# Optimization experiments

Hardware: AMD Instinct MI355X
Metric: run time of the kernel (lower is better)

## Reference

```python
import jax, jax.numpy as jnp
import numpy as np

B, N, C, H = 4, 2048, 1024, 16
D = C // H  # head_dim = 64


def setup_inputs() -> dict:
    key = jax.random.key(0)
    ks = jax.random.split(key, 11)
    s = 1.0 / np.sqrt(C)
    return {
        "query": jax.random.normal(ks[0], (B, N, C), jnp.float32),
        "key": jax.random.normal(ks[1], (B, N, C), jnp.float32),
        "value": jax.random.normal(ks[2], (B, N, C), jnp.float32),
        "Wq": jax.random.normal(ks[3], (C, C), jnp.float32) * s,
        "bq": jax.random.normal(ks[4], (C,), jnp.float32) * s,
        "Wk": jax.random.normal(ks[5], (C, C), jnp.float32) * s,
        "bk": jax.random.normal(ks[6], (C,), jnp.float32) * s,
        "Wv": jax.random.normal(ks[7], (C, C), jnp.float32) * s,
        "bv": jax.random.normal(ks[8], (C,), jnp.float32) * s,
        "Wp": jax.random.normal(ks[9], (C, C), jnp.float32) * s,
        "bp": jax.random.normal(ks[10], (C,), jnp.float32) * s,
    }


def _split_heads(x):
    # [B, N, C] -> [B, H, N, D]
    return x.reshape(B, N, H, D).transpose(0, 2, 1, 3)


def reference(query, key, value, Wq, bq, Wk, bk, Wv, bv, Wp, bp):
    q = _split_heads(query @ Wq + bq)  # [B,H,N,D]
    k = _split_heads(key @ Wk + bk)
    v = _split_heads(value @ Wv + bv)

    # custom additive frequency bias over key positions (broadcast over B,H,Tq)
    freq_range = jnp.linspace(0.0, 1.0, N, dtype=query.dtype)
    freq_bias = -((freq_range - 0.5) ** 2) * 10.0  # [N]

    scale = 1.0 / jnp.sqrt(jnp.asarray(D, query.dtype))
    att = jnp.einsum('bhqd,bhkd->bhqk', q * scale, k)  # [B,H,N,N]
    att = att + freq_bias[None, None, None, :]
    att = jax.nn.softmax(att, axis=-1)
    y = jnp.einsum('bhqk,bhkd->bhqd', att, v)  # [B,H,N,D]

    y = y.transpose(0, 2, 1, 3).reshape(B, N, C)
    out = y @ Wp + bp
    return out
```

## Files before the change

kernel.cpp:

```cpp
#include <hip/hip_runtime.h>
#include <stdint.h>

typedef unsigned short u16;
typedef float f32x4 __attribute__((ext_vector_type(4)));
typedef float f32x16 __attribute__((ext_vector_type(16)));
typedef __bf16 bf16x8 __attribute__((ext_vector_type(8)));
typedef u16 u16x8 __attribute__((ext_vector_type(8)));
typedef u16 u16x4 __attribute__((ext_vector_type(4)));

#define B_ 4
#define N_ 2048
#define C_ 1024
#define H_ 16
#define D_ 64

__device__ __forceinline__ u16 f2bf(float f) {
  unsigned u = __builtin_bit_cast(unsigned, f);
  u += 0x7FFFu + ((u >> 16) & 1u);
  return (u16)(u >> 16);
}
__device__ __forceinline__ float bf2f(u16 h) {
  unsigned u = ((unsigned)h) << 16;
  return __builtin_bit_cast(float, u);
}
__device__ __forceinline__ f32x4 mfma16(u16x8 a, u16x8 b, f32x4 c) {
  return __builtin_amdgcn_mfma_f32_16x16x32_bf16(
      __builtin_bit_cast(bf16x8, a), __builtin_bit_cast(bf16x8, b), c, 0, 0, 0);
}
__device__ __forceinline__ f32x16 mfma32(u16x8 a, u16x8 b, f32x16 c) {
  return __builtin_amdgcn_mfma_f32_32x32x16_bf16(
      __builtin_bit_cast(bf16x8, a), __builtin_bit_cast(bf16x8, b), c, 0, 0, 0);
}
__device__ __forceinline__ void gload_lds16(const void* g, void* l) {
  __builtin_amdgcn_global_load_lds(
      (const __attribute__((address_space(1))) void*)g,
      (__attribute__((address_space(3))) void*)l, 16, 0, 0);
}
__device__ __forceinline__ float exp2_hw(float x) {
  return __builtin_amdgcn_exp2f(x);
}
__device__ __forceinline__ unsigned cvt_pk_bf16(float lo, float hi) {
  unsigned d;
  asm("v_cvt_pk_bf16_f32 %0, %1, %2" : "=v"(d) : "v"(lo), "v"(hi));
  return d;
}

__global__ __launch_bounds__(256) void convert_x(const float* __restrict__ in,
                                                 u16* __restrict__ out, int n4) {
  int i = blockIdx.x * 256 + threadIdx.x;
  if (i >= n4) return;
  f32x4 v = *(const f32x4*)(in + (size_t)i * 4);
  u16x4 o;
#pragma unroll
  for (int j = 0; j < 4; j++) o[j] = f2bf(v[j]);
  *(u16x4*)(out + (size_t)i * 4) = o;
}

__global__ __launch_bounds__(256) void transpose_convert_w(const float* __restrict__ in,
                                                           u16* __restrict__ out) {
  __shared__ float tile[64][65];
  const int t = threadIdx.x;
  const int bx = blockIdx.x;
  const int tr = (bx >> 4) << 6;
  const int tc = (bx & 15) << 6;
#pragma unroll
  for (int i = 0; i < 16; i++) {
    int idx = i * 256 + t;
    int rr = idx >> 6, cc = idx & 63;
    tile[rr][cc] = in[(size_t)(tr + rr) * C_ + tc + cc];
  }
  __syncthreads();
#pragma unroll
  for (int i = 0; i < 16; i++) {
    int idx = i * 256 + t;
    int rr = idx >> 6, cc = idx & 63;
    out[(size_t)(tc + rr) * C_ + tr + cc] = f2bf(tile[cc][rr]);
  }
}

template <int EPI, bool SPLIT>
__global__ __launch_bounds__(256) void gemm128(
    const u16* __restrict__ A, const u16* __restrict__ A2,
    const u16* __restrict__ BT, const float* __restrict__ bias,
    void* __restrict__ outp, float scale, int M, int N, int K) {
  __shared__ u16 lA[128 * 32];
  __shared__ u16 lB[128 * 32];
  __shared__ u16 lA2[SPLIT ? 128 * 32 : 8];

  const int t = threadIdx.x;
  const int w = t >> 6;
  const int lane = t & 63;
  const int g = lane >> 4;
  const int r = lane & 15;
  const int nTn = N >> 7;
  const int tm = blockIdx.x / nTn;
  const int tn = blockIdx.x % nTn;
  const int m0 = tm << 7;
  const int n0 = tn << 7;
  const int wm = (w >> 1) << 6;
  const int wn = (w & 1) << 6;

  const int row_s = t >> 2;
  const int kc_s = (t & 3) << 3;

  f32x4 acc[4][4] = {};

  for (int k0 = 0; k0 < K; k0 += 32) {
    __syncthreads();
    {
      const u16* gA = A + (size_t)(m0 + row_s) * K + (k0 + kc_s);
      gload_lds16(gA, (char*)lA + (w << 10));
      gload_lds16(gA + (size_t)64 * K, (char*)lA + 4096 + (w << 10));
      const u16* gB = BT + (size_t)(n0 + row_s) * K + (k0 + kc_s);
      gload_lds16(gB, (char*)lB + (w << 10));
      gload_lds16(gB + (size_t)64 * K, (char*)lB + 4096 + (w << 10));
      if constexpr (SPLIT) {
        const u16* gA2 = A2 + (size_t)(m0 + row_s) * K + (k0 + kc_s);
        gload_lds16(gA2, (char*)lA2 + (w << 10));
        gload_lds16(gA2 + (size_t)64 * K, (char*)lA2 + 4096 + (w << 10));
      }
    }
    asm volatile("s_waitcnt vmcnt(0)" ::: "memory");
    __syncthreads();

    u16x8 af[4], bfv[4];
#pragma unroll
    for (int i = 0; i < 4; i++)
      af[i] = *(const u16x8*)&lA[(wm + i * 16 + r) * 32 + g * 8];
#pragma unroll
    for (int i = 0; i < 4; i++)
      bfv[i] = *(const u16x8*)&lB[(wn + i * 16 + r) * 32 + g * 8];
#pragma unroll
    for (int mi = 0; mi < 4; mi++)
#pragma unroll
      for (int ni = 0; ni < 4; ni++)
        acc[mi][ni] = mfma16(af[mi], bfv[ni], acc[mi][ni]);
    if constexpr (SPLIT) {
      u16x8 al[4];
#pragma unroll
      for (int i = 0; i < 4; i++)
        al[i] = *(const u16x8*)&lA2[(wm + i * 16 + r) * 32 + g * 8];
#pragma unroll
      for (int mi = 0; mi < 4; mi++)
#pragma unroll
        for (int ni = 0; ni < 4; ni++)
          acc[mi][ni] = mfma16(al[mi], bfv[ni], acc[mi][ni]);
    }
  }

  float bv[4];
#pragma unroll
  for (int ni = 0; ni < 4; ni++) bv[ni] = bias[n0 + wn + ni * 16 + r];

  if constexpr (EPI == 2) {
    float* out = (float*)outp;
#pragma unroll
    for (int mi = 0; mi < 4; mi++)
#pragma unroll
      for (int ni = 0; ni < 4; ni++)
#pragma unroll
        for (int j = 0; j < 4; j++) {
          int gm = m0 + wm + mi * 16 + g * 4 + j;
          int gn = n0 + wn + ni * 16 + r;
          out[(size_t)gm * N + gn] = (acc[mi][ni][j] + bv[ni]) * scale;
        }
  } else if constexpr (EPI == 0) {
    u16* out = (u16*)outp;
#pragma unroll
    for (int mi = 0; mi < 4; mi++)
#pragma unroll
      for (int ni = 0; ni < 4; ni++)
#pragma unroll
        for (int j = 0; j < 4; j++) {
          int gm = m0 + wm + mi * 16 + g * 4 + j;
          int gn = n0 + wn + ni * 16 + r;
          float v = (acc[mi][ni][j] + bv[ni]) * scale;
          int b = gm >> 11, n = gm & 2047, h = gn >> 6, d = gn & 63;
          out[((((size_t)b * H_ + h) * N_ + n) << 6) + d] = f2bf(v);
        }
  } else if constexpr (EPI == 3) {
    u16* out = (u16*)outp;
#pragma unroll
    for (int mi = 0; mi < 4; mi++)
#pragma unroll
      for (int ni = 0; ni < 4; ni++)
#pragma unroll
        for (int j = 0; j < 4; j++) {
          int gm = m0 + wm + mi * 16 + g * 4 + j;
          int gn = n0 + wn + ni * 16 + r;
          float v = acc[mi][ni][j] + bv[ni];
          int b = gm >> 11, n = gm & 2047, h = gn >> 6, d = gn & 63;
          size_t off = (((size_t)(b * H_ + h)) << 17) + ((size_t)(n >> 5) << 11) +
                       ((d >> 4) << 9) + ((((d >> 3) & 1) << 5) + (n & 31)) * 8 + (d & 7);
          out[off] = f2bf(v);
        }
  } else {
    u16* out = (u16*)outp;
#pragma unroll
    for (int mi = 0; mi < 4; mi++)
#pragma unroll
      for (int ni = 0; ni < 4; ni++) {
        int gm0 = m0 + wm + mi * 16 + g * 4;
        int gn = n0 + wn + ni * 16 + r;
        int b = gm0 >> 11, n = gm0 & 2047, h = gn >> 6, d = gn & 63;
        size_t off = (((size_t)(b * H_ + h)) << 17) + ((size_t)(n >> 6) << 12) +
                     ((size_t)((d >> 5) * 4 + ((n >> 4) & 3)) << 9) +
                     ((((n >> 3) & 1) << 5) + (d & 31)) * 8 + (n & 7);
        u16x4 pk;
#pragma unroll
        for (int j = 0; j < 4; j++) pk[j] = f2bf(acc[mi][ni][j] + bv[ni]);
        *(u16x4*)&out[off] = pk;
      }
  }
}

__device__ __forceinline__ void load_kv(const u16* __restrict__ Kb,
                                        const u16* __restrict__ Vb, int k0,
                                        int lane, u16x8 (&kf)[8], u16x8 (&vf)[8]) {
  const u16* pK = Kb + ((size_t)(k0 >> 5) << 11) + lane * 8;
#pragma unroll
  for (int s = 0; s < 4; s++) {
    kf[s] = *(const u16x8*)(pK + (s << 9));
    kf[4 + s] = *(const u16x8*)(pK + 2048 + (s << 9));
  }
  const u16* pV = Vb + ((size_t)(k0 >> 6) << 12) + lane * 8;
#pragma unroll
  for (int c = 0; c < 8; c++) vf[c] = *(const u16x8*)(pV + (c << 9));
}

__device__ __forceinline__ void attn_tile(int k0, const float* __restrict__ tbl,
                                          float* __restrict__ xlds,
                                          const u16x8 (&kf)[8], const u16x8 (&vf)[8],
                                          const u16x8 (&qf)[4], f32x16& o0, f32x16& o1,
                                          float& m_e, float& l_run, int ql, int h) {
  const float L2E = 1.44269504088896340736f;
  f32x16 st0 = {}, st1 = {};
#pragma unroll
  for (int s = 0; s < 4; s++) st0 = mfma32(kf[s], qf[s], st0);
#pragma unroll
  for (int s = 0; s < 4; s++) st1 = mfma32(kf[4 + s], qf[s], st1);

  float e0[16], e1[16];
#pragma unroll
  for (int g2 = 0; g2 < 4; g2++) {
    f32x4 t0 = *(const f32x4*)&tbl[k0 + 8 * g2 + 4 * h];
    f32x4 t1 = *(const f32x4*)&tbl[k0 + 32 + 8 * g2 + 4 * h];
#pragma unroll
    for (int jj = 0; jj < 4; jj++) {
      e0[g2 * 4 + jj] = fmaf(st0[g2 * 4 + jj], L2E, t0[jj]);
      e1[g2 * 4 + jj] = fmaf(st1[g2 * 4 + jj], L2E, t1[jj]);
    }
  }
  float mx[8];
#pragma unroll
  for (int j = 0; j < 8; j++)
    mx[j] = fmaxf(fmaxf(e0[j], e0[j + 8]), fmaxf(e1[j], e1[j + 8]));
#pragma unroll
  for (int j = 0; j < 4; j++) mx[j] = fmaxf(mx[j], mx[j + 4]);
  float pmax = fmaxf(fmaxf(mx[0], mx[1]), fmaxf(mx[2], mx[3]));
  pmax = fmaxf(pmax, __shfl_xor(pmax, 32));

  if (!__all(pmax <= m_e + 8.0f)) {
    float m_new = fmaxf(m_e, pmax);
    float resc = exp2_hw(m_e - m_new);
    xlds[ql] = resc;
#pragma unroll
    for (int g2 = 0; g2 < 4; g2++) {
      f32x4 r4 = *(const f32x4*)&xlds[8 * g2 + 4 * h];
#pragma unroll
      for (int jj = 0; jj < 4; jj++) {
        o0[g2 * 4 + jj] *= r4[jj];
        o1[g2 * 4 + jj] *= r4[jj];
      }
    }
    l_run *= resc;
    m_e = m_new;
  }

#pragma unroll
  for (int j = 0; j < 16; j++) e0[j] = exp2_hw(e0[j] - m_e);
#pragma unroll
  for (int j = 0; j < 16; j++) e1[j] = exp2_hw(e1[j] - m_e);
  float sm[8];
#pragma unroll
  for (int j = 0; j < 8; j++) sm[j] = (e0[j] + e0[j + 8]) + (e1[j] + e1[j + 8]);
#pragma unroll
  for (int j = 0; j < 4; j++) sm[j] += sm[j + 4];
  float lt = (sm[0] + sm[1]) + (sm[2] + sm[3]);
  lt += __shfl_xor(lt, 32);
  l_run += lt;

  unsigned W0[8], W1[8];
#pragma unroll
  for (int j = 0; j < 8; j++) {
    W0[j] = cvt_pk_bf16(e0[2 * j], e0[2 * j + 1]);
    W1[j] = cvt_pk_bf16(e1[2 * j], e1[2 * j + 1]);
  }
  u16x8 pa[4];
#pragma unroll
  for (int c = 0; c < 2; c++) {
    unsigned a0 = W0[4 * c], b0 = W0[4 * c + 2];
    unsigned a1 = W0[4 * c + 1], b1 = W0[4 * c + 3];
    asm("v_permlane32_swap_b32 %0, %1" : "+v"(a0), "+v"(b0));
    asm("v_permlane32_swap_b32 %0, %1" : "+v"(a1), "+v"(b1));
    union { unsigned u[4]; u16x8 v; } pk_;
    pk_.u[0] = a0; pk_.u[1] = a1; pk_.u[2] = b0; pk_.u[3] = b1;
    pa[c] = pk_.v;
  }
#pragma unroll
  for (int c = 0; c < 2; c++) {
    unsigned a0 = W1[4 * c], b0 = W1[4 * c + 2];
    unsigned a1 = W1[4 * c + 1], b1 = W1[4 * c + 3];
    asm("v_permlane32_swap_b32 %0, %1" : "+v"(a0), "+v"(b0));
    asm("v_permlane32_swap_b32 %0, %1" : "+v"(a1), "+v"(b1));
    union { unsigned u[4]; u16x8 v; } pk_;
    pk_.u[0] = a0; pk_.u[1] = a1; pk_.u[2] = b0; pk_.u[3] = b1;
    pa[2 + c] = pk_.v;
  }

#pragma unroll
  for (int cc = 0; cc < 4; cc++) {
    o0 = mfma32(pa[cc], vf[cc], o0);
    o1 = mfma32(pa[cc], vf[4 + cc], o1);
  }
}

__global__ __launch_bounds__(256) void attn_fwd(
    const u16* __restrict__ Q, const u16* __restrict__ K,
    const u16* __restrict__ VT, u16* __restrict__ yhi, u16* __restrict__ ylo) {
  __shared__ __align__(16) float tbl[N_];
  __shared__ __align__(16) float xldsa[4][32];

  const int bid0 = blockIdx.x;
  const int bid = (bid0 & 7) * 128 + (bid0 >> 3);
  const int bh = bid >> 4;
  const int qt = bid & 15;
  const int t = threadIdx.x, w = t >> 6, lane = t & 63;
  const int ql = lane & 31;
  const int h = lane >> 5;
  const float L2E = 1.44269504088896340736f;

#pragma unroll
  for (int i = 0; i < 8; i++) {
    int k = i * 256 + t;
    float tt = (float)k * (1.0f / 2047.0f) - 0.5f;
    tbl[k] = -10.0f * L2E * tt * tt;
  }
  __syncthreads();

  const int q0 = qt * 128 + w * 32;
  const u16* Qb = Q + (size_t)bh * (N_ * D_);
  const u16* Kb = K + (size_t)bh * (N_ * D_);
  const u16* Vb = VT + (size_t)bh * (D_ * N_);
  float* xlds = xldsa[w];

  u16x8 qf[4];
#pragma unroll
  for (int s = 0; s < 4; s++)
    qf[s] = *(const u16x8*)(Qb + (size_t)(q0 + ql) * D_ + s * 16 + h * 8);

  f32x16 o0 = {}, o1 = {};
  float m_e = -INFINITY, l_run = 0.f;

  u16x8 kA[8], vA[8], kB[8], vB[8];
  load_kv(Kb, Vb, 0, lane, kA, vA);

  for (int k0 = 0; k0 < N_; k0 += 128) {
    load_kv(Kb, Vb, k0 + 64, lane, kB, vB);
    attn_tile(k0, tbl, xlds, kA, vA, qf, o0, o1, m_e, l_run, ql, h);
    if (k0 + 128 < N_)
      load_kv(Kb, Vb, k0 + 128, lane, kA, vA);
    attn_tile(k0 + 64, tbl, xlds, kB, vB, qf, o0, o1, m_e, l_run, ql, h);
  }

  float linv = 1.0f / l_run;
  xlds[ql] = linv;
  const int b = bh >> 4, hh = bh & 15;
#pragma unroll
  for (int g2 = 0; g2 < 4; g2++) {
    f32x4 r4 = *(const f32x4*)&xlds[8 * g2 + 4 * h];
#pragma unroll
    for (int jj = 0; jj < 4; jj++) {
      int q = q0 + 8 * g2 + 4 * h + jj;
      size_t base = ((size_t)b * N_ + q) * C_ + hh * 64;
      float v0 = o0[g2 * 4 + jj] * r4[jj];
      float v1 = o1[g2 * 4 + jj] * r4[jj];
      u16 h0 = f2bf(v0), h1 = f2bf(v1);
      yhi[base + ql] = h0;
      ylo[base + ql] = f2bf(v0 - bf2f(h0));
      yhi[base + 32 + ql] = h1;
      ylo[base + 32 + ql] = f2bf(v1 - bf2f(h1));
    }
  }
}

extern "C" void kernel_launch(void* const* d_in, const int* in_sizes, int n_in,
                              void* d_out, int out_size, void* d_ws, size_t ws_size,
                              hipStream_t stream) {
  (void)in_sizes; (void)n_in; (void)out_size; (void)ws_size;
  const float* q_in = (const float*)d_in[0];
  const float* k_in = (const float*)d_in[1];
  const float* v_in = (const float*)d_in[2];
  const float* Wq = (const float*)d_in[3];
  const float* bq = (const float*)d_in[4];
  const float* Wk = (const float*)d_in[5];
  const float* bk = (const float*)d_in[6];
  const float* Wv = (const float*)d_in[7];
  const float* bv = (const float*)d_in[8];
  const float* Wp = (const float*)d_in[9];
  const float* bp = (const float*)d_in[10];

  char* ws = (char*)d_ws;
  const size_t SZ_X = (size_t)8192 * 1024 * sizeof(u16);
  const size_t SZ_W = (size_t)1024 * 1024 * sizeof(u16);
  u16* Xq = (u16*)(ws);
  u16* Xk = (u16*)(ws + SZ_X);
  u16* Xv = (u16*)(ws + 2 * SZ_X);
  u16* Qb = (u16*)(ws + 3 * SZ_X);
  u16* Kb = (u16*)(ws + 4 * SZ_X);
  u16* VT = (u16*)(ws + 5 * SZ_X);
  u16* WqT = (u16*)(ws + 6 * SZ_X);
  u16* WkT = (u16*)(ws + 6 * SZ_X + SZ_W);
  u16* WvT = (u16*)(ws + 6 * SZ_X + 2 * SZ_W);
  u16* WpT = (u16*)(ws + 6 * SZ_X + 3 * SZ_W);
  u16* Yhi = Xq;
  u16* Ylo = Xk;

  convert_x<<<8192, 256, 0, stream>>>(q_in, Xq, 2097152);
  convert_x<<<8192, 256, 0, stream>>>(k_in, Xk, 2097152);
  convert_x<<<8192, 256, 0, stream>>>(v_in, Xv, 2097152);
  transpose_convert_w<<<256, 256, 0, stream>>>(Wq, WqT);
  transpose_convert_w<<<256, 256, 0, stream>>>(Wk, WkT);
  transpose_convert_w<<<256, 256, 0, stream>>>(Wv, WvT);
  transpose_convert_w<<<256, 256, 0, stream>>>(Wp, WpT);

  gemm128<0, false><<<512, 256, 0, stream>>>(Xq, nullptr, WqT, bq, Qb, 0.125f, 8192, 1024, 1024);
  gemm128<3, false><<<512, 256, 0, stream>>>(Xk, nullptr, WkT, bk, Kb, 1.0f, 8192, 1024, 1024);
  gemm128<1, false><<<512, 256, 0, stream>>>(Xv, nullptr, WvT, bv, VT, 1.0f, 8192, 1024, 1024);

  attn_fwd<<<1024, 256, 0, stream>>>(Qb, Kb, VT, Yhi, Ylo);

  gemm128<2, true><<<512, 256, 0, stream>>>(Yhi, Ylo, WpT, bp, (float*)d_out, 1.0f, 8192, 1024, 1024);
}
```

Measured before the change: 292.5 us.

## Double GEMM K-tile to 64 with XOR-swizzled LDS and batch conversion launches

The projection GEMM now stages a 64-wide K slice per iteration instead of 32. This halves the number of barrier and wait cycles per output tile and gives more MFMA work per sync. The LDS layout uses an XOR swizzle on 16-byte chunks to avoid bank conflicts on the wider 128-byte rows. The input conversion and weight transpose kernels are also merged into single multi-plane launches (3 and 4 planes) to cut launch count. The cost is more LDS per block, which may reduce occupancy for the split variant.

```diff
diff --git a/kernel.cpp b/kernel.cpp
--- a/kernel.cpp
+++ b/kernel.cpp
@@ -45,10 +45,13 @@
   return d;
 }
 
-__global__ __launch_bounds__(256) void convert_x(const float* __restrict__ in,
-                                                 u16* __restrict__ out, int n4) {
+__global__ __launch_bounds__(256) void convert_x3(
+    const float* __restrict__ a, const float* __restrict__ b,
+    const float* __restrict__ c, u16* __restrict__ oa, u16* __restrict__ ob,
+    u16* __restrict__ oc) {
+  const float* in = blockIdx.y == 0 ? a : (blockIdx.y == 1 ? b : c);
+  u16* out = blockIdx.y == 0 ? oa : (blockIdx.y == 1 ? ob : oc);
   int i = blockIdx.x * 256 + threadIdx.x;
-  if (i >= n4) return;
   f32x4 v = *(const f32x4*)(in + (size_t)i * 4);
   u16x4 o;
 #pragma unroll
@@ -56,8 +59,15 @@
   *(u16x4*)(out + (size_t)i * 4) = o;
 }
 
-__global__ __launch_bounds__(256) void transpose_convert_w(const float* __restrict__ in,
-                                                           u16* __restrict__ out) {
+__global__ __launch_bounds__(256) void transpose_convert_w4(
+    const float* __restrict__ w0, const float* __restrict__ w1,
+    const float* __restrict__ w2, const float* __restrict__ w3,
+    u16* __restrict__ o0, u16* __restrict__ o1, u16* __restrict__ o2,
+    u16* __restrict__ o3) {
+  const float* in = blockIdx.y == 0 ? w0
+                    : blockIdx.y == 1 ? w1
+                    : blockIdx.y == 2 ? w2 : w3;
+  u16* out = blockIdx.y == 0 ? o0 : blockIdx.y == 1 ? o1 : blockIdx.y == 2 ? o2 : o3;
   __shared__ float tile[64][65];
   const int t = threadIdx.x;
   const int bx = blockIdx.x;
@@ -83,9 +93,9 @@
     const u16* __restrict__ A, const u16* __restrict__ A2,
     const u16* __restrict__ BT, const float* __restrict__ bias,
     void* __restrict__ outp, float scale, int M, int N, int K) {
-  __shared__ u16 lA[128 * 32];
-  __shared__ u16 lB[128 * 32];
-  __shared__ u16 lA2[SPLIT ? 128 * 32 : 8];
+  __shared__ u16 lA[128 * 64];
+  __shared__ u16 lB[128 * 64];
+  __shared__ u16 lA2[SPLIT ? 128 * 64 : 8];
 
   const int t = threadIdx.x;
   const int w = t >> 6;
@@ -100,51 +110,66 @@
   const int wm = (w >> 1) << 6;
   const int wn = (w & 1) << 6;
 
-  const int row_s = t >> 2;
-  const int kc_s = (t & 3) << 3;
+  const int srow = t >> 3;
+  const int scol = ((t & 7) ^ (srow & 7)) << 3;
 
   f32x4 acc[4][4] = {};
 
-  for (int k0 = 0; k0 < K; k0 += 32) {
+  for (int k0 = 0; k0 < K; k0 += 64) {
     __syncthreads();
     {
-      const u16* gA = A + (size_t)(m0 + row_s) * K + (k0 + kc_s);
-      gload_lds16(gA, (char*)lA + (w << 10));
-      gload_lds16(gA + (size_t)64 * K, (char*)lA + 4096 + (w << 10));
-      const u16* gB = BT + (size_t)(n0 + row_s) * K + (k0 + kc_s);
-      gload_lds16(gB, (char*)lB + (w << 10));
-      gload_lds16(gB + (size_t)64 * K, (char*)lB + 4096 + (w << 10));
+      const u16* gA = A + (size_t)(m0 + srow) * K + (k0 + scol);
+      const u16* gB = BT + (size_t)(n0 + srow) * K + (k0 + scol);
+#pragma unroll
+      for (int p = 0; p < 4; p++) {
+        gload_lds16(gA + (size_t)(p * 32) * K, (char*)lA + (p << 12) + (w << 10));
+        gload_lds16(gB + (size_t)(p * 32) * K, (char*)lB + (p << 12) + (w << 10));
+      }
       if constexpr (SPLIT) {
-        const u16* gA2 = A2 + (size_t)(m0 + row_s) * K + (k0 + kc_s);
-        gload_lds16(gA2, (char*)lA2 + (w << 10));
-        gload_lds16(gA2 + (size_t)64 * K, (char*)lA2 + 4096 + (w << 10));
+        const u16* gA2 = A2 + (size_t)(m0 + srow) * K + (k0 + scol);
+#pragma unroll
+        for (int p = 0; p < 4; p++)
+          gload_lds16(gA2 + (size_t)(p * 32) * K, (char*)lA2 + (p << 12) + (w << 10));
       }
     }
     asm volatile("s_waitcnt vmcnt(0)" ::: "memory");
     __syncthreads();
 
-    u16x8 af[4], bfv[4];
-#pragma unroll
-    for (int i = 0; i < 4; i++)
-      af[i] = *(const u16x8*)&lA[(wm + i * 16 + r) * 32 + g * 8];
-#pragma unroll
-    for (int i = 0; i < 4; i++)
-      bfv[i] = *(const u16x8*)&lB[(wn + i * 16 + r) * 32 + g * 8];
-#pragma unroll
-    for (int mi = 0; mi < 4; mi++)
-#pragma unroll
-      for (int ni = 0; ni < 4; ni++)
-        acc[mi][ni] = mfma16(af[mi], bfv[ni], acc[mi][ni]);
-    if constexpr (SPLIT) {
-      u16x8 al[4];
-#pragma unroll
-      for (int i = 0; i < 4; i++)
-        al[i] = *(const u16x8*)&lA2[(wm + i * 16 + r) * 32 + g * 8];
+    const int rx = (r & 7) << 4;
+#pragma unroll
+    for (int kk = 0; kk < 2; kk++) {
+      u16x8 af[4], bfv[4];
+#pragma unroll
+      for (int i = 0; i < 4; i++) {
+        int rowa = wm + i * 16 + r;
+        af[i] = *(const u16x8*)((const char*)lA + (rowa << 7) +
+                                (((kk << 6) + (g << 4)) ^ rx));
+      }
+#pragma unroll
+      for (int i = 0; i < 4; i++) {
+        int rowb = wn + i * 16 + r;
+        bfv[i] = *(const u16x8*)((const char*)lB + (rowb << 7) +
+                                 (((kk << 6) + (g << 4)) ^ rx));
+      }
 #pragma unroll
       for (int mi = 0; mi < 4; mi++)
 #pragma unroll
         for (int ni = 0; ni < 4; ni++)
-          acc[mi][ni] = mfma16(al[mi], bfv[ni], acc[mi][ni]);
+          acc[mi][ni] = mfma16(af[mi], bfv[ni], acc[mi][ni]);
+      if constexpr (SPLIT) {
+        u16x8 al[4];
+#pragma unroll
+        for (int i = 0; i < 4; i++) {
+          int rowa = wm + i * 16 + r;
+          al[i] = *(const u16x8*)((const char*)lA2 + (rowa << 7) +
+                                  (((kk << 6) + (g << 4)) ^ rx));
+        }
+#pragma unroll
+        for (int mi = 0; mi < 4; mi++)
+#pragma unroll
+          for (int ni = 0; ni < 4; ni++)
+            acc[mi][ni] = mfma16(al[mi], bfv[ni], acc[mi][ni]);
+      }
     }
   }
 
@@ -426,13 +451,9 @@
   u16* Yhi = Xq;
   u16* Ylo = Xk;
 
-  convert_x<<<8192, 256, 0, stream>>>(q_in, Xq, 2097152);
-  convert_x<<<8192, 256, 0, stream>>>(k_in, Xk, 2097152);
-  convert_x<<<8192, 256, 0, stream>>>(v_in, Xv, 2097152);
-  transpose_convert_w<<<256, 256, 0, stream>>>(Wq, WqT);
-  transpose_convert_w<<<256, 256, 0, stream>>>(Wk, WkT);
-  transpose_convert_w<<<256, 256, 0, stream>>>(Wv, WvT);
-  transpose_convert_w<<<256, 256, 0, stream>>>(Wp, WpT);
+  convert_x3<<<dim3(8192, 3), 256, 0, stream>>>(q_in, k_in, v_in, Xq, Xk, Xv);
+  transpose_convert_w4<<<dim3(256, 4), 256, 0, stream>>>(Wq, Wk, Wv, Wp, WqT, WkT,
+                                                         WvT, WpT);
 
   gemm128<0, false><<<512, 256, 0, stream>>>(Xq, nullptr, WqT, bq, Qb, 0.125f, 8192, 1024, 1024);
   gemm128<3, false><<<512, 256, 0, stream>>>(Xk, nullptr, WkT, bk, Kb, 1.0f, 8192, 1024, 1024);
```

New measurement: 272.0 us. 7.0% less time.
